# Kernel tuning notes

Hardware: AMD Instinct MI355X
Metric: run time of the kernel (lower is better)

The kernel has to match this reference:

```python
import jax, jax.numpy as jnp
import numpy as np

N_EMBD = 1024
N_HEAD = 16
HEAD_DIM = N_EMBD // N_HEAD
HIDDEN = int(2 * N_EMBD * 4 / 3)  # 2730, SwiGLU sizing from source
EPS = 1e-5


def setup_inputs() -> dict:
    key = jax.random.key(0)
    ks = jax.random.split(key, 16)
    def lin(k, fan_in, fan_out):
        bound = 1.0 / np.sqrt(fan_in)
        return jax.random.uniform(k, (fan_in, fan_out), jnp.float32, -bound, bound)
    return {
        "x": jax.random.normal(ks[0], (2, 2048, N_EMBD), jnp.float32),
        "ln1_g": jnp.ones((N_EMBD,), jnp.float32),
        "ln1_b": jnp.zeros((N_EMBD,), jnp.float32),
        "qkv_w": lin(ks[1], N_EMBD, 3 * N_EMBD),
        "qkv_b": jnp.zeros((3 * N_EMBD,), jnp.float32),
        "proj_w": lin(ks[2], N_EMBD, N_EMBD),
        "proj_b": jnp.zeros((N_EMBD,), jnp.float32),
        "ln2_g": jnp.ones((N_EMBD,), jnp.float32),
        "ln2_b": jnp.zeros((N_EMBD,), jnp.float32),
        "gate_w": lin(ks[3], N_EMBD, HIDDEN),
        "gate_b": jnp.zeros((HIDDEN,), jnp.float32),
        "up_w": lin(ks[4], N_EMBD, HIDDEN),
        "up_b": jnp.zeros((HIDDEN,), jnp.float32),
        "down_w": lin(ks[5], HIDDEN, N_EMBD),
        "down_b": jnp.zeros((N_EMBD,), jnp.float32),
    }


def _layernorm(x, g, b):
    mu = jnp.mean(x, axis=-1, keepdims=True)
    var = jnp.mean(jnp.square(x - mu), axis=-1, keepdims=True)
    return (x - mu) * jax.lax.rsqrt(var + EPS) * g + b


def _alibi_slopes(n_heads):
    i = jnp.arange(1, n_heads + 1, dtype=jnp.float32)
    return 1.0 / jnp.power(2.0, 8.0 * i / n_heads)  # [H]


def reference(x, ln1_g, ln1_b, qkv_w, qkv_b, proj_w, proj_b,
              ln2_g, ln2_b, gate_w, gate_b, up_w, up_b, down_w, down_b):
    B, T, C = x.shape
    residual = x
    h = _layernorm(x, ln1_g, ln1_b)
    qkv = h @ qkv_w + qkv_b  # [B,T,3C]
    q, k, v = jnp.split(qkv, 3, axis=-1)
    q = q.reshape(B, T, N_HEAD, HEAD_DIM).transpose(0, 2, 1, 3)
    k = k.reshape(B, T, N_HEAD, HEAD_DIM).transpose(0, 2, 1, 3)
    v = v.reshape(B, T, N_HEAD, HEAD_DIM).transpose(0, 2, 1, 3)
    scale = 1.0 / np.sqrt(HEAD_DIM)
    attn = jnp.einsum('bhqd,bhkd->bhqk', q, k) * scale
    # ALiBi: slope * |q_pos - k_pos| (abs distance, as in source)
    pos = jnp.arange(T)
    dist = jnp.abs(pos[None, :] - pos[:, None]).astype(jnp.float32)  # [T,T]
    slopes = _alibi_slopes(N_HEAD)  # [H]
    attn = attn + slopes[None, :, None, None] * dist[None, None, :, :]
    causal = pos[:, None] >= pos[None, :]  # tril mask
    attn = jnp.where(causal[None, None], attn, -jnp.inf)
    attn = jax.nn.softmax(attn, axis=-1)
    out = jnp.einsum('bhqk,bhkd->bhqd', attn, v)
    out = out.transpose(0, 2, 1, 3).reshape(B, T, C)
    out = out @ proj_w + proj_b
    x = residual + out
    residual = x
    h = _layernorm(x, ln2_g, ln2_b)
    gate = h @ gate_w + gate_b
    up = h @ up_w + up_b
    ff = (gate * jax.nn.sigmoid(gate) * up) @ down_w + down_b
    return residual + ff
```

## Files before the change

kernel.cpp:

```cpp
#include <hip/hip_runtime.h>
#include <cstdint>
#include <cstddef>

#define T_SEQ   2048
#define BATCH   2
#define NEMBD   1024
#define NHEAD   16
#define HDIM    64
#define HIDDEN  2730
#define HIDDENP 2816
#define MROWS   4096

typedef __bf16 bf16x8 __attribute__((ext_vector_type(8)));
typedef __bf16 bf16x4 __attribute__((ext_vector_type(4)));
typedef float  f32x4  __attribute__((ext_vector_type(4)));

__device__ __forceinline__ void gl2lds16(const void* g, void* l) {
    __builtin_amdgcn_global_load_lds((const __attribute__((address_space(1))) void*)g,
                                     (__attribute__((address_space(3))) void*)l, 16, 0, 0);
}

__global__ __launch_bounds__(256) void conv_trans(const float* __restrict__ W,
                                                  __bf16* __restrict__ Wt,
                                                  int K, int N, int Kp)
{
    __shared__ float tile[32][33];
    const int n0 = blockIdx.x * 32, k0 = blockIdx.y * 32;
    const int tx = threadIdx.x, ty = threadIdx.y;
#pragma unroll
    for (int i = ty; i < 32; i += 8) {
        int k = k0 + i, n = n0 + tx;
        tile[i][tx] = (k < K && n < N) ? W[(size_t)k * N + n] : 0.f;
    }
    __syncthreads();
#pragma unroll
    for (int i = ty; i < 32; i += 8) {
        int n = n0 + i, k = k0 + tx;
        Wt[(size_t)n * Kp + k] = (__bf16)tile[tx][i];
    }
}

__global__ __launch_bounds__(256) void ln_kernel(const float* __restrict__ x,
                                                 const float* __restrict__ g,
                                                 const float* __restrict__ b,
                                                 __bf16* __restrict__ out)
{
    const int row = blockIdx.x;
    const int t   = threadIdx.x;
    const float4 v = ((const float4*)(x + (size_t)row * NEMBD))[t];
    float s  = v.x + v.y + v.z + v.w;
    float sq = v.x * v.x + v.y * v.y + v.z * v.z + v.w * v.w;
#pragma unroll
    for (int d = 1; d < 64; d <<= 1) { s += __shfl_xor(s, d); sq += __shfl_xor(sq, d); }
    __shared__ float ssh[4], sqsh[4];
    const int w = t >> 6;
    if ((t & 63) == 0) { ssh[w] = s; sqsh[w] = sq; }
    __syncthreads();
    s  = ssh[0] + ssh[1] + ssh[2] + ssh[3];
    sq = sqsh[0] + sqsh[1] + sqsh[2] + sqsh[3];
    const float mean = s * (1.f / NEMBD);
    const float var  = sq * (1.f / NEMBD) - mean * mean;
    const float rstd = rsqrtf(var + 1e-5f);
    const float4 gg = ((const float4*)g)[t];
    const float4 bb = ((const float4*)b)[t];
    bf16x4 o;
    o[0] = (__bf16)((v.x - mean) * rstd * gg.x + bb.x);
    o[1] = (__bf16)((v.y - mean) * rstd * gg.y + bb.y);
    o[2] = (__bf16)((v.z - mean) * rstd * gg.z + bb.z);
    o[3] = (__bf16)((v.w - mean) * rstd * gg.w + bb.w);
    *(bf16x4*)&out[(size_t)row * NEMBD + t * 4] = o;
}

template <int MODE>
__global__ __launch_bounds__(256) void gemm_bt(const __bf16* __restrict__ A,
                                               const __bf16* __restrict__ Bt,
                                               const float* __restrict__ bias, int Nreal,
                                               const float* __restrict__ res,
                                               const __bf16* __restrict__ gbuf,
                                               void* __restrict__ outp,
                                               void* __restrict__ outp2,
                                               int Kp, int N)
{
    __shared__ alignas(16) __bf16 Ash[128 * 32];
    __shared__ alignas(16) __bf16 Bsh[128 * 32];
    const int tid  = threadIdx.x;
    const int w    = tid >> 6, l = tid & 63;
    const int ln   = l & 15, quad = l >> 4;
    const int wm   = w >> 1, wn = w & 1;
    const long m0  = (long)blockIdx.y * 128;
    const long n0  = (long)blockIdx.x * 128;
    f32x4 acc[4][4] = {};
    const __bf16* Ab = A + m0 * Kp;
    const __bf16* Bb = Bt + n0 * Kp;
    const int arow = l >> 2, acol = (l & 3) * 8;

    for (int k0 = 0; k0 < Kp; k0 += 32) {
#pragma unroll
        for (int it = 0; it < 2; ++it) {
            const int c = w * 2 + it;
            gl2lds16(Ab + (long)(c * 16 + arow) * Kp + k0 + acol, Ash + c * 512);
            gl2lds16(Bb + (long)(c * 16 + arow) * Kp + k0 + acol, Bsh + c * 512);
        }
        __syncthreads();
        bf16x8 af[4], bfr[4];
#pragma unroll
        for (int i = 0; i < 4; ++i) {
            af[i]  = *(const bf16x8*)&Ash[(wm * 64 + i * 16 + ln) * 32 + quad * 8];
            bfr[i] = *(const bf16x8*)&Bsh[(wn * 64 + i * 16 + ln) * 32 + quad * 8];
        }
#pragma unroll
        for (int tm = 0; tm < 4; ++tm)
#pragma unroll
            for (int tn = 0; tn < 4; ++tn)
                acc[tm][tn] = __builtin_amdgcn_mfma_f32_16x16x32_bf16(af[tm], bfr[tn], acc[tm][tn], 0, 0, 0);
        __syncthreads();
    }

    if (MODE == 3 && n0 >= 2048) {
        __bf16* vt = (__bf16*)outp2;
        const long bbq    = m0 >> 11;
        const long t0base = (m0 & 2047) + wm * 64;
#pragma unroll
        for (int tm = 0; tm < 4; ++tm)
#pragma unroll
            for (int tn = 0; tn < 4; ++tn) {
                const long col = n0 + wn * 64 + tn * 16 + ln;
                const float bv = bias[col];
                bf16x4 pv;
#pragma unroll
                for (int r = 0; r < 4; ++r) pv[r] = (__bf16)(acc[tm][tn][r] + bv);
                const long tt = t0base + tm * 16 + quad * 4;
                *(bf16x4*)&vt[(bbq * 1024 + (col - 2048)) * 2048 + tt] = pv;
            }
        return;
    }

#pragma unroll
    for (int tm = 0; tm < 4; ++tm)
#pragma unroll
        for (int tn = 0; tn < 4; ++tn) {
            const long col = n0 + wn * 64 + tn * 16 + ln;
            const float bv = (col < Nreal) ? bias[col] : 0.f;
#pragma unroll
            for (int r = 0; r < 4; ++r) {
                const long row = m0 + wm * 64 + tm * 16 + quad * 4 + r;
                float v = acc[tm][tn][r] + bv;
                if (MODE == 0) {
                    ((__bf16*)outp)[row * N + col] = (__bf16)v;
                } else if (MODE == 2) {
                    const float gg = (float)gbuf[row * N + col];
                    const float sg = gg / (1.f + __expf(-gg));
                    ((__bf16*)outp)[row * N + col] = (__bf16)(sg * v);
                } else {
                    ((__bf16*)outp)[row * 2048 + col] = (__bf16)v;
                }
            }
        }
}

__global__ __launch_bounds__(256) void gemm_bt_h(const __bf16* __restrict__ A,
                                                 const __bf16* __restrict__ Bt,
                                                 const float* __restrict__ bias,
                                                 const float* __restrict__ res,
                                                 float* __restrict__ outp, int Kp, int N)
{
    __shared__ alignas(16) __bf16 Ash[64 * 32];
    __shared__ alignas(16) __bf16 Bsh[128 * 32];
    const int tid  = threadIdx.x;
    const int w    = tid >> 6, l = tid & 63;
    const int ln   = l & 15, quad = l >> 4;
    const int wm   = w >> 1, wn = w & 1;
    const long m0  = (long)blockIdx.y * 64;
    const long n0  = (long)blockIdx.x * 128;
    f32x4 acc[2][4] = {};
    const __bf16* Ab = A + m0 * Kp;
    const __bf16* Bb = Bt + n0 * Kp;
    const int arow = l >> 2, acol = (l & 3) * 8;

    for (int k0 = 0; k0 < Kp; k0 += 32) {
        gl2lds16(Ab + (long)(w * 16 + arow) * Kp + k0 + acol, Ash + w * 512);
#pragma unroll
        for (int it = 0; it < 2; ++it) {
            const int c = w * 2 + it;
            gl2lds16(Bb + (long)(c * 16 + arow) * Kp + k0 + acol, Bsh + c * 512);
        }
        __syncthreads();
        bf16x8 af[2], bfr[4];
#pragma unroll
        for (int i = 0; i < 2; ++i)
            af[i] = *(const bf16x8*)&Ash[(wm * 32 + i * 16 + ln) * 32 + quad * 8];
#pragma unroll
        for (int i = 0; i < 4; ++i)
            bfr[i] = *(const bf16x8*)&Bsh[(wn * 64 + i * 16 + ln) * 32 + quad * 8];
#pragma unroll
        for (int tm = 0; tm < 2; ++tm)
#pragma unroll
            for (int tn = 0; tn < 4; ++tn)
                acc[tm][tn] = __builtin_amdgcn_mfma_f32_16x16x32_bf16(af[tm], bfr[tn], acc[tm][tn], 0, 0, 0);
        __syncthreads();
    }

#pragma unroll
    for (int tm = 0; tm < 2; ++tm)
#pragma unroll
        for (int tn = 0; tn < 4; ++tn) {
            const long col = n0 + wn * 64 + tn * 16 + ln;
            const float bv = bias[col];
#pragma unroll
            for (int r = 0; r < 4; ++r) {
                const long row = m0 + wm * 32 + tm * 16 + quad * 4 + r;
                outp[row * N + col] = acc[tm][tn][r] + bv + res[row * N + col];
            }
        }
}

__device__ __forceinline__ void attn_stage(const __bf16* __restrict__ qk,
                                           const __bf16* __restrict__ vT,
                                           __bf16* Kd, __bf16* Vd,
                                           long bT, int bb, int hh, int k0, int w, int l)
{
#pragma unroll
    for (int jj = 0; jj < 2; ++jj) {
        const int j   = w * 2 + jj;
        const int row = j * 8 + (l >> 3);
        const int seg = (l & 7) ^ (row & 7);
        gl2lds16(qk + (bT + k0 + row) * 2048 + 1024 + hh * 64 + seg * 8, Kd + j * 512);
        gl2lds16(vT + ((long)(bb * 1024 + hh * 64 + row)) * 2048 + k0 + seg * 8, Vd + j * 512);
    }
}

__global__ __launch_bounds__(256, 4) void attn_kernel(const __bf16* __restrict__ qk,
                                                      const __bf16* __restrict__ vT,
                                                      __bf16* __restrict__ out)
{
    __shared__ alignas(16) __bf16 Ksh[2][64 * 64];
    __shared__ alignas(16) __bf16 Vtsh[2][64 * 64];
    __shared__ alignas(16) __bf16 Psh[4][16 * 64];

    const int tid = threadIdx.x;
    const int w   = tid >> 6, l = tid & 63;
    const int ln  = l & 15, quad = l >> 4;
    const int bh  = blockIdx.x;
    const int qt  = 31 - blockIdx.y;
    const int bb  = bh >> 4, hh = bh & 15;
    const long bT = (long)bb * T_SEQ;
    const int q0b = qt * 64;
    const int q0w = q0b + w * 16;
    const float slope = exp2f(-0.5f * (float)(hh + 1));
    const float c1  = 0.125f * 1.44269504089f;
    const float sl2 = slope * 1.44269504089f;

    bf16x8 qf0, qf1;
    {
        const __bf16* qp = qk + (bT + q0w + ln) * 2048 + hh * 64 + quad * 8;
        qf0 = *(const bf16x8*)qp;
        qf1 = *(const bf16x8*)(qp + 32);
    }
    bf16x8 onesf;
#pragma unroll
    for (int j = 0; j < 8; ++j) onesf[j] = (__bf16)1.0f;

    f32x4 o[4] = {};
    f32x4 oS = {};

    const int sw  = ln & 7;
    const int nch = qt + 1;

    attn_stage(qk, vT, Ksh[0], Vtsh[0], bT, bb, hh, 0, w, l);

    for (int i = 0; i < nch; ++i) {
        const int k0  = i * 64;
        const int cur = i & 1;
        if (i + 1 < nch) {
            attn_stage(qk, vT, Ksh[cur ^ 1], Vtsh[cur ^ 1], bT, bb, hh, k0 + 64, w, l);
            asm volatile("s_waitcnt vmcnt(4)" ::: "memory");
        } else {
            asm volatile("s_waitcnt vmcnt(0)" ::: "memory");
        }
        __builtin_amdgcn_s_barrier();

        f32x4 s[4];
#pragma unroll
        for (int kt = 0; kt < 4; ++kt) s[kt] = (f32x4){0.f, 0.f, 0.f, 0.f};
#pragma unroll
        for (int kt = 0; kt < 4; ++kt) {
            bf16x8 kf;
            kf = *(const bf16x8*)&Ksh[cur][(kt * 16 + ln) * 64 + ((quad ^ sw) << 3)];
            s[kt] = __builtin_amdgcn_mfma_f32_16x16x32_bf16(qf0, kf, s[kt], 0, 0, 0);
            kf = *(const bf16x8*)&Ksh[cur][(kt * 16 + ln) * 64 + (((4 + quad) ^ sw) << 3)];
            s[kt] = __builtin_amdgcn_mfma_f32_16x16x32_bf16(qf1, kf, s[kt], 0, 0, 0);
        }

        const float tk0 = -sl2 * (float)(k0 + ln);
        float tk[4];
#pragma unroll
        for (int kt = 0; kt < 4; ++kt) tk[kt] = tk0 - sl2 * (float)(kt * 16);
        const bool full = (k0 + 64 <= q0w);
#pragma unroll
        for (int r = 0; r < 4; ++r) {
            const int qrow = q0w + quad * 4 + r;
#pragma unroll
            for (int kt = 0; kt < 4; ++kt) {
                float e = exp2f(fmaf(s[kt][r], c1, tk[kt]));
                if (!full) e = (k0 + kt * 16 + ln <= qrow) ? e : 0.f;
                s[kt][r] = e;
            }
        }

#pragma unroll
        for (int kt = 0; kt < 4; ++kt)
#pragma unroll
            for (int r = 0; r < 4; ++r) {
                const int q = quad * 4 + r;
                Psh[w][q * 64 + (((kt * 2 + (ln >> 3)) ^ (q & 7)) << 3) + (ln & 7)] = (__bf16)s[kt][r];
            }
        asm volatile("s_waitcnt lgkmcnt(0)" ::: "memory");
#pragma unroll
        for (int kh2 = 0; kh2 < 2; ++kh2) {
            const bf16x8 pfr = *(const bf16x8*)&Psh[w][ln * 64 + (((kh2 * 4 + quad) ^ sw) << 3)];
#pragma unroll
            for (int dt = 0; dt < 4; ++dt) {
                const bf16x8 vf = *(const bf16x8*)&Vtsh[cur][(dt * 16 + ln) * 64 + (((kh2 * 4 + quad) ^ sw) << 3)];
                o[dt] = __builtin_amdgcn_mfma_f32_16x16x32_bf16(pfr, vf, o[dt], 0, 0, 0);
            }
            oS = __builtin_amdgcn_mfma_f32_16x16x32_bf16(pfr, onesf, oS, 0, 0, 0);
        }
        __builtin_amdgcn_s_barrier();
    }

    float rl[4];
#pragma unroll
    for (int r = 0; r < 4; ++r) rl[r] = 1.0f / oS[r];
#pragma unroll
    for (int dt = 0; dt < 4; ++dt)
#pragma unroll
        for (int r = 0; r < 4; ++r) {
            const long row = bT + q0w + quad * 4 + r;
            out[row * NEMBD + hh * 64 + dt * 16 + ln] = (__bf16)(o[dt][r] * rl[r]);
        }
}

extern "C" void kernel_launch(void* const* d_in, const int* in_sizes, int n_in,
                              void* d_out, int out_size, void* d_ws, size_t ws_size,
                              hipStream_t stream)
{
    const float* x      = (const float*)d_in[0];
    const float* ln1_g  = (const float*)d_in[1];
    const float* ln1_b  = (const float*)d_in[2];
    const float* qkv_w  = (const float*)d_in[3];
    const float* qkv_b  = (const float*)d_in[4];
    const float* proj_w = (const float*)d_in[5];
    const float* proj_b = (const float*)d_in[6];
    const float* ln2_g  = (const float*)d_in[7];
    const float* ln2_b  = (const float*)d_in[8];
    const float* gate_w = (const float*)d_in[9];
    const float* gate_b = (const float*)d_in[10];
    const float* up_w   = (const float*)d_in[11];
    const float* up_b   = (const float*)d_in[12];
    const float* down_w = (const float*)d_in[13];
    const float* down_b = (const float*)d_in[14];
    float* out = (float*)d_out;
    char*  ws  = (char*)d_ws;

    const size_t OFF_WQKV  = 0;
    const size_t OFF_WPROJ = 6291456;
    const size_t OFF_WGATE = 8388608;
    const size_t OFF_WUP   = 14155776;
    const size_t OFF_WDOWN = 19922944;
    const size_t OFF_H     = 25690112;
    const size_t OFF_QK    = 34078720;
    const size_t OFF_VT    = 50855936;
    const size_t OFF_G     = OFF_QK;
    const size_t OFF_ATTN  = 59244544;
    const size_t OFF_FF    = 67633152;
    const size_t NEED      = 90701824;
    if (ws_size < NEED) return;

    __bf16* wqkv  = (__bf16*)(ws + OFF_WQKV);
    __bf16* wproj = (__bf16*)(ws + OFF_WPROJ);
    __bf16* wgate = (__bf16*)(ws + OFF_WGATE);
    __bf16* wup   = (__bf16*)(ws + OFF_WUP);
    __bf16* wdown = (__bf16*)(ws + OFF_WDOWN);
    __bf16* hbuf  = (__bf16*)(ws + OFF_H);
    __bf16* qkb   = (__bf16*)(ws + OFF_QK);
    __bf16* vtb   = (__bf16*)(ws + OFF_VT);
    __bf16* gbuf  = (__bf16*)(ws + OFF_G);
    __bf16* attnb = (__bf16*)(ws + OFF_ATTN);
    __bf16* ffbuf = (__bf16*)(ws + OFF_FF);

    const dim3 tb(32, 8);
    conv_trans<<<dim3(96, 32), tb, 0, stream>>>(qkv_w,  wqkv,  1024, 3072, 1024);
    conv_trans<<<dim3(32, 32), tb, 0, stream>>>(proj_w, wproj, 1024, 1024, 1024);
    conv_trans<<<dim3(88, 32), tb, 0, stream>>>(gate_w, wgate, 1024, HIDDEN, 1024);
    conv_trans<<<dim3(88, 32), tb, 0, stream>>>(up_w,   wup,   1024, HIDDEN, 1024);
    conv_trans<<<dim3(32, 88), tb, 0, stream>>>(down_w, wdown, HIDDEN, 1024, HIDDENP);

    ln_kernel<<<MROWS, 256, 0, stream>>>(x, ln1_g, ln1_b, hbuf);
    gemm_bt<3><<<dim3(24, 32), 256, 0, stream>>>(hbuf, wqkv, qkv_b, 3072, nullptr, nullptr, qkb, vtb, 1024, 3072);
    attn_kernel<<<dim3(32, 32), 256, 0, stream>>>(qkb, vtb, attnb);
    gemm_bt_h<<<dim3(8, 64), 256, 0, stream>>>(attnb, wproj, proj_b, x, out, 1024, 1024);
    ln_kernel<<<MROWS, 256, 0, stream>>>(out, ln2_g, ln2_b, hbuf);
    gemm_bt<0><<<dim3(22, 32), 256, 0, stream>>>(hbuf, wgate, gate_b, HIDDEN, nullptr, nullptr, gbuf, nullptr, 1024, HIDDENP);
    gemm_bt<2><<<dim3(22, 32), 256, 0, stream>>>(hbuf, wup, up_b, HIDDEN, nullptr, gbuf, ffbuf, nullptr, 1024, HIDDENP);
    gemm_bt_h<<<dim3(8, 64), 256, 0, stream>>>(ffbuf, wdown, down_b, out, out, HIDDENP, 1024);
}
```

Baseline: 409.5 us.

## Fuse gate/up GEMMs with SwiGLU epilogue and double-buffer LDS in GEMMs

New measurement: 401.5 us. 1.02x faster.

```diff
diff --git a/kernel.cpp b/kernel.cpp
--- a/kernel.cpp
+++ b/kernel.cpp
@@ -71,18 +71,15 @@
     *(bf16x4*)&out[(size_t)row * NEMBD + t * 4] = o;
 }
 
-template <int MODE>
-__global__ __launch_bounds__(256) void gemm_bt(const __bf16* __restrict__ A,
-                                               const __bf16* __restrict__ Bt,
-                                               const float* __restrict__ bias, int Nreal,
-                                               const float* __restrict__ res,
-                                               const __bf16* __restrict__ gbuf,
-                                               void* __restrict__ outp,
-                                               void* __restrict__ outp2,
-                                               int Kp, int N)
-{
-    __shared__ alignas(16) __bf16 Ash[128 * 32];
-    __shared__ alignas(16) __bf16 Bsh[128 * 32];
+__global__ __launch_bounds__(256) void gemm_qkv(const __bf16* __restrict__ A,
+                                                const __bf16* __restrict__ Bt,
+                                                const float* __restrict__ bias,
+                                                __bf16* __restrict__ qkout,
+                                                __bf16* __restrict__ vtout,
+                                                int Kp)
+{
+    __shared__ alignas(16) __bf16 Ash[2][128 * 32];
+    __shared__ alignas(16) __bf16 Bsh[2][128 * 32];
     const int tid  = threadIdx.x;
     const int w    = tid >> 6, l = tid & 63;
     const int ln   = l & 15, quad = l >> 4;
@@ -94,30 +91,41 @@
     const __bf16* Bb = Bt + n0 * Kp;
     const int arow = l >> 2, acol = (l & 3) * 8;
 
-    for (int k0 = 0; k0 < Kp; k0 += 32) {
+    auto stage = [&](int buf, int k0) {
 #pragma unroll
         for (int it = 0; it < 2; ++it) {
             const int c = w * 2 + it;
-            gl2lds16(Ab + (long)(c * 16 + arow) * Kp + k0 + acol, Ash + c * 512);
-            gl2lds16(Bb + (long)(c * 16 + arow) * Kp + k0 + acol, Bsh + c * 512);
-        }
-        __syncthreads();
+            gl2lds16(Ab + (long)(c * 16 + arow) * Kp + k0 + acol, &Ash[buf][c * 512]);
+            gl2lds16(Bb + (long)(c * 16 + arow) * Kp + k0 + acol, &Bsh[buf][c * 512]);
+        }
+    };
+
+    const int nk = Kp >> 5;
+    stage(0, 0);
+    for (int kt = 0; kt < nk; ++kt) {
+        const int cur = kt & 1;
+        if (kt + 1 < nk) {
+            stage(cur ^ 1, (kt + 1) * 32);
+            asm volatile("s_waitcnt vmcnt(4)" ::: "memory");
+        } else {
+            asm volatile("s_waitcnt vmcnt(0)" ::: "memory");
+        }
+        __builtin_amdgcn_s_barrier();
         bf16x8 af[4], bfr[4];
 #pragma unroll
         for (int i = 0; i < 4; ++i) {
-            af[i]  = *(const bf16x8*)&Ash[(wm * 64 + i * 16 + ln) * 32 + quad * 8];
-            bfr[i] = *(const bf16x8*)&Bsh[(wn * 64 + i * 16 + ln) * 32 + quad * 8];
+            af[i]  = *(const bf16x8*)&Ash[cur][(wm * 64 + i * 16 + ln) * 32 + quad * 8];
+            bfr[i] = *(const bf16x8*)&Bsh[cur][(wn * 64 + i * 16 + ln) * 32 + quad * 8];
         }
 #pragma unroll
         for (int tm = 0; tm < 4; ++tm)
 #pragma unroll
             for (int tn = 0; tn < 4; ++tn)
                 acc[tm][tn] = __builtin_amdgcn_mfma_f32_16x16x32_bf16(af[tm], bfr[tn], acc[tm][tn], 0, 0, 0);
-        __syncthreads();
-    }
-
-    if (MODE == 3 && n0 >= 2048) {
-        __bf16* vt = (__bf16*)outp2;
+        __builtin_amdgcn_s_barrier();
+    }
+
+    if (n0 >= 2048) {
         const long bbq    = m0 >> 11;
         const long t0base = (m0 & 2047) + wm * 64;
 #pragma unroll
@@ -130,30 +138,106 @@
 #pragma unroll
                 for (int r = 0; r < 4; ++r) pv[r] = (__bf16)(acc[tm][tn][r] + bv);
                 const long tt = t0base + tm * 16 + quad * 4;
-                *(bf16x4*)&vt[(bbq * 1024 + (col - 2048)) * 2048 + tt] = pv;
+                *(bf16x4*)&vtout[(bbq * 1024 + (col - 2048)) * 2048 + tt] = pv;
             }
         return;
     }
-
 #pragma unroll
     for (int tm = 0; tm < 4; ++tm)
 #pragma unroll
         for (int tn = 0; tn < 4; ++tn) {
             const long col = n0 + wn * 64 + tn * 16 + ln;
-            const float bv = (col < Nreal) ? bias[col] : 0.f;
+            const float bv = bias[col];
 #pragma unroll
             for (int r = 0; r < 4; ++r) {
                 const long row = m0 + wm * 64 + tm * 16 + quad * 4 + r;
-                float v = acc[tm][tn][r] + bv;
-                if (MODE == 0) {
-                    ((__bf16*)outp)[row * N + col] = (__bf16)v;
-                } else if (MODE == 2) {
-                    const float gg = (float)gbuf[row * N + col];
-                    const float sg = gg / (1.f + __expf(-gg));
-                    ((__bf16*)outp)[row * N + col] = (__bf16)(sg * v);
-                } else {
-                    ((__bf16*)outp)[row * 2048 + col] = (__bf16)v;
-                }
+                qkout[row * 2048 + col] = (__bf16)(acc[tm][tn][r] + bv);
+            }
+        }
+}
+
+__global__ __launch_bounds__(256) void gemm_gateup(const __bf16* __restrict__ A,
+                                                   const __bf16* __restrict__ Bg_,
+                                                   const __bf16* __restrict__ Bu_,
+                                                   const float* __restrict__ gbias,
+                                                   const float* __restrict__ ubias,
+                                                   __bf16* __restrict__ outp)
+{
+    __shared__ alignas(16) __bf16 Ash[2][128 * 32];
+    __shared__ alignas(16) __bf16 Bgs[2][128 * 32];
+    __shared__ alignas(16) __bf16 Bus[2][128 * 32];
+    const int Kp = 1024;
+    const int tid  = threadIdx.x;
+    const int w    = tid >> 6, l = tid & 63;
+    const int ln   = l & 15, quad = l >> 4;
+    const int wm   = w >> 1, wn = w & 1;
+    const long m0  = (long)blockIdx.y * 128;
+    const long n0  = (long)blockIdx.x * 128;
+    f32x4 accg[4][4] = {}, accu[4][4] = {};
+    const __bf16* Ab  = A   + m0 * Kp;
+    const __bf16* Bgb = Bg_ + n0 * Kp;
+    const __bf16* Bub = Bu_ + n0 * Kp;
+    const int arow = l >> 2, acol = (l & 3) * 8;
+
+    auto stage = [&](int buf, int k0) {
+#pragma unroll
+        for (int it = 0; it < 2; ++it) {
+            const int c = w * 2 + it;
+            gl2lds16(Ab  + (long)(c * 16 + arow) * Kp + k0 + acol, &Ash[buf][c * 512]);
+            gl2lds16(Bgb + (long)(c * 16 + arow) * Kp + k0 + acol, &Bgs[buf][c * 512]);
+            gl2lds16(Bub + (long)(c * 16 + arow) * Kp + k0 + acol, &Bus[buf][c * 512]);
+        }
+    };
+
+    const int nk = Kp >> 5;
+    stage(0, 0);
+    for (int kt = 0; kt < nk; ++kt) {
+        const int cur = kt & 1;
+        if (kt + 1 < nk) {
+            stage(cur ^ 1, (kt + 1) * 32);
+            asm volatile("s_waitcnt vmcnt(6)" ::: "memory");
+        } else {
+            asm volatile("s_waitcnt vmcnt(0)" ::: "memory");
+        }
+        __builtin_amdgcn_s_barrier();
+        bf16x8 af[4], bfr[4];
+#pragma unroll
+        for (int i = 0; i < 4; ++i)
+            af[i] = *(const bf16x8*)&Ash[cur][(wm * 64 + i * 16 + ln) * 32 + quad * 8];
+#pragma unroll
+        for (int i = 0; i < 4; ++i)
+            bfr[i] = *(const bf16x8*)&Bgs[cur][(wn * 64 + i * 16 + ln) * 32 + quad * 8];
+#pragma unroll
+        for (int tm = 0; tm < 4; ++tm)
+#pragma unroll
+            for (int tn = 0; tn < 4; ++tn)
+                accg[tm][tn] = __builtin_amdgcn_mfma_f32_16x16x32_bf16(af[tm], bfr[tn], accg[tm][tn], 0, 0, 0);
+#pragma unroll
+        for (int i = 0; i < 4; ++i)
+            bfr[i] = *(const bf16x8*)&Bus[cur][(wn * 64 + i * 16 + ln) * 32 + quad * 8];
+#pragma unroll
+        for (int tm = 0; tm < 4; ++tm)
+#pragma unroll
+            for (int tn = 0; tn < 4; ++tn)
+                accu[tm][tn] = __builtin_amdgcn_mfma_f32_16x16x32_bf16(af[tm], bfr[tn], accu[tm][tn], 0, 0, 0);
+        __builtin_amdgcn_s_barrier();
+    }
+
+#pragma unroll
+    for (int tm = 0; tm < 4; ++tm)
+#pragma unroll
+        for (int tn = 0; tn < 4; ++tn) {
+            const long col = n0 + wn * 64 + tn * 16 + ln;
+            const bool real = (col < HIDDEN);
+            const float gb = real ? gbias[col] : 0.f;
+            const float ub = real ? ubias[col] : 0.f;
+#pragma unroll
+            for (int r = 0; r < 4; ++r) {
+                const long row = m0 + wm * 64 + tm * 16 + quad * 4 + r;
+                const float gv = accg[tm][tn][r] + gb;
+                const float uv = accu[tm][tn][r] + ub;
+                const float sg = gv / (1.f + __expf(-gv));
+                outp[row * HIDDENP + col] = (__bf16)(sg * uv);
             }
         }
 }
@@ -164,8 +248,8 @@
                                                  const float* __restrict__ res,
                                                  float* __restrict__ outp, int Kp, int N)
 {
-    __shared__ alignas(16) __bf16 Ash[64 * 32];
-    __shared__ alignas(16) __bf16 Bsh[128 * 32];
+    __shared__ alignas(16) __bf16 Ash[2][64 * 32];
+    __shared__ alignas(16) __bf16 Bsh[2][128 * 32];
     const int tid  = threadIdx.x;
     const int w    = tid >> 6, l = tid & 63;
     const int ln   = l & 15, quad = l >> 4;
@@ -177,27 +261,39 @@
     const __bf16* Bb = Bt + n0 * Kp;
     const int arow = l >> 2, acol = (l & 3) * 8;
 
-    for (int k0 = 0; k0 < Kp; k0 += 32) {
-        gl2lds16(Ab + (long)(w * 16 + arow) * Kp + k0 + acol, Ash + w * 512);
+    auto stage = [&](int buf, int k0) {
+        gl2lds16(Ab + (long)(w * 16 + arow) * Kp + k0 + acol, &Ash[buf][w * 512]);
 #pragma unroll
         for (int it = 0; it < 2; ++it) {
             const int c = w * 2 + it;
-            gl2lds16(Bb + (long)(c * 16 + arow) * Kp + k0 + acol, Bsh + c * 512);
-        }
-        __syncthreads();
+            gl2lds16(Bb + (long)(c * 16 + arow) * Kp + k0 + acol, &Bsh[buf][c * 512]);
+        }
+    };
+
+    const int nk = Kp >> 5;
+    stage(0, 0);
+    for (int kt = 0; kt < nk; ++kt) {
+        const int cur = kt & 1;
+        if (kt + 1 < nk) {
+            stage(cur ^ 1, (kt + 1) * 32);
+            asm volatile("s_waitcnt vmcnt(3)" ::: "memory");
+        } else {
+            asm volatile("s_waitcnt vmcnt(0)" ::: "memory");
+        }
+        __builtin_amdgcn_s_barrier();
         bf16x8 af[2], bfr[4];
 #pragma unroll
         for (int i = 0; i < 2; ++i)
-            af[i] = *(const bf16x8*)&Ash[(wm * 32 + i * 16 + ln) * 32 + quad * 8];
+            af[i] = *(const bf16x8*)&Ash[cur][(wm * 32 + i * 16 + ln) * 32 + quad * 8];
 #pragma unroll
         for (int i = 0; i < 4; ++i)
-            bfr[i] = *(const bf16x8*)&Bsh[(wn * 64 + i * 16 + ln) * 32 + quad * 8];
+            bfr[i] = *(const bf16x8*)&Bsh[cur][(wn * 64 + i * 16 + ln) * 32 + quad * 8];
 #pragma unroll
         for (int tm = 0; tm < 2; ++tm)
 #pragma unroll
             for (int tn = 0; tn < 4; ++tn)
                 acc[tm][tn] = __builtin_amdgcn_mfma_f32_16x16x32_bf16(af[tm], bfr[tn], acc[tm][tn], 0, 0, 0);
-        __syncthreads();
+        __builtin_amdgcn_s_barrier();
     }
 
 #pragma unroll
@@ -370,7 +466,6 @@
     const size_t OFF_H     = 25690112;
     const size_t OFF_QK    = 34078720;
     const size_t OFF_VT    = 50855936;
-    const size_t OFF_G     = OFF_QK;
     const size_t OFF_ATTN  = 59244544;
     const size_t OFF_FF    = 67633152;
     const size_t NEED      = 90701824;
@@ -384,7 +479,6 @@
     __bf16* hbuf  = (__bf16*)(ws + OFF_H);
     __bf16* qkb   = (__bf16*)(ws + OFF_QK);
     __bf16* vtb   = (__bf16*)(ws + OFF_VT);
-    __bf16* gbuf  = (__bf16*)(ws + OFF_G);
     __bf16* attnb = (__bf16*)(ws + OFF_ATTN);
     __bf16* ffbuf = (__bf16*)(ws + OFF_FF);
 
@@ -396,11 +490,10 @@
     conv_trans<<<dim3(32, 88), tb, 0, stream>>>(down_w, wdown, HIDDEN, 1024, HIDDENP);
 
     ln_kernel<<<MROWS, 256, 0, stream>>>(x, ln1_g, ln1_b, hbuf);
-    gemm_bt<3><<<dim3(24, 32), 256, 0, stream>>>(hbuf, wqkv, qkv_b, 3072, nullptr, nullptr, qkb, vtb, 1024, 3072);
+    gemm_qkv<<<dim3(24, 32), 256, 0, stream>>>(hbuf, wqkv, qkv_b, qkb, vtb, 1024);
     attn_kernel<<<dim3(32, 32), 256, 0, stream>>>(qkb, vtb, attnb);
     gemm_bt_h<<<dim3(8, 64), 256, 0, stream>>>(attnb, wproj, proj_b, x, out, 1024, 1024);
     ln_kernel<<<MROWS, 256, 0, stream>>>(out, ln2_g, ln2_b, hbuf);
-    gemm_bt<0><<<dim3(22, 32), 256, 0, stream>>>(hbuf, wgate, gate_b, HIDDEN, nullptr, nullptr, gbuf, nullptr, 1024, HIDDENP);
-    gemm_bt<2><<<dim3(22, 32), 256, 0, stream>>>(hbuf, wup, up_b, HIDDEN, nullptr, gbuf, ffbuf, nullptr, 1024, HIDDENP);
+    gemm_gateup<<<dim3(22, 32), 256, 0, stream>>>(hbuf, wgate, wup, gate_b, up_b, ffbuf);
     gemm_bt_h<<<dim3(8, 64), 256, 0, stream>>>(ffbuf, wdown, down_b, out, out, HIDDENP, 1024);
 }
```
